# Kernel optimization log

Hardware: AMD Instinct MI355X
Metric: run time of the kernel (lower is better)

## Reference

```python
import jax, jax.numpy as jnp
import numpy as np

INDIM = 1024
NHEADS = 16
DK = INDIM // NHEADS  # 64
DV = INDIM // NHEADS  # 64
B, S = 4, 2048


def setup_inputs() -> dict:
    key = jax.random.key(0)
    ks = jax.random.split(key, 5)
    x = jax.random.normal(ks[0], (B, S, INDIM), dtype=jnp.float32)
    std_qk = np.sqrt(2.0 / (INDIM + DK)).astype(np.float32)
    std_v = np.sqrt(2.0 / (INDIM + DV)).astype(np.float32)
    Wq = jax.random.normal(ks[1], (NHEADS * DK, INDIM), dtype=jnp.float32) * std_qk
    Wk = jax.random.normal(ks[2], (NHEADS * DK, INDIM), dtype=jnp.float32) * std_qk
    Wv = jax.random.normal(ks[3], (NHEADS * DV, INDIM), dtype=jnp.float32) * std_v
    # xavier normal for output proj
    std_o = np.sqrt(2.0 / (NHEADS * DV + INDIM)).astype(np.float32)
    Wo = jax.random.normal(ks[4], (INDIM, NHEADS * DV), dtype=jnp.float32) * std_o
    bq = jnp.zeros((NHEADS * DK,), jnp.float32)
    bk = jnp.zeros((NHEADS * DK,), jnp.float32)
    bv = jnp.zeros((NHEADS * DV,), jnp.float32)
    bo = jnp.zeros((INDIM,), jnp.float32)
    return {"x": x, "Wq": Wq, "bq": bq, "Wk": Wk, "bk": bk, "Wv": Wv, "bv": bv, "Wo": Wo, "bo": bo}


def reference(x, Wq, bq, Wk, bk, Wv, bv, Wo, bo):
    b, s, _ = x.shape
    q = (x @ Wq.T + bq).reshape(b, s, NHEADS, DK)
    k = (x @ Wk.T + bk).reshape(b, s, NHEADS, DK)
    v = (x @ Wv.T + bv).reshape(b, s, NHEADS, DV)
    # scores: [b, h, s, z]
    w = jnp.einsum('bshd,bzhd->bhsz', q, k)
    # original divides by sqrt(d_v) (v.size(-1)) when scale=True
    w = w / jnp.sqrt(jnp.float32(DV))
    w = jax.nn.softmax(w, axis=-1)
    vw = jnp.einsum('bhsz,bzhd->bshd', w, v)  # [b, s, h, dv]
    vw = vw.reshape(b, s, NHEADS * DV)
    out = vw @ Wo.T + bo
    return out
```

## Files before the change

kernel.cpp:

```cpp
#include <hip/hip_runtime.h>
#include <hip/hip_bf16.h>
#include <cstdint>
#include <cstddef>

#define NHEADS 16
#define HDIM   64
#define SEQ    2048
#define BATCH  4
#define IND    1024
#define MTOT   (BATCH*SEQ)

typedef __attribute__((ext_vector_type(8))) short bf16x8;
typedef __attribute__((ext_vector_type(8))) _Float16 f16x8;
typedef __attribute__((ext_vector_type(2))) _Float16 f16x2;
typedef __attribute__((ext_vector_type(4))) float f32x4;
typedef __attribute__((ext_vector_type(16))) float f32x16;
typedef __attribute__((ext_vector_type(2))) int i32x2;
typedef __attribute__((ext_vector_type(4))) unsigned u32x4;

#if __has_builtin(__builtin_amdgcn_exp2f)
#define EXP2(x) __builtin_amdgcn_exp2f(x)
#else
#define EXP2(x) exp2f(x)
#endif

__device__ __forceinline__ unsigned short f2b(float f) {
  unsigned u = __builtin_bit_cast(unsigned, f);
  u += 0x7FFFu + ((u >> 16) & 1u);
  return (unsigned short)(u >> 16);
}
__device__ __forceinline__ unsigned cvt2(float lo, float hi) {
  float2 t; t.x = lo; t.y = hi;
  __hip_bfloat162 h = __float22bfloat162_rn(t);
  const unsigned short ulo = __bfloat16_as_ushort(h.x);
  const unsigned short uhi = __bfloat16_as_ushort(h.y);
  return (unsigned)ulo | ((unsigned)uhi << 16);
}
__device__ __forceinline__ float m3(float a, float b, float c) {
  return fmaxf(fmaxf(a, b), c);
}

__device__ __forceinline__ void gload_lds16(const void* g, void* l) {
  __builtin_amdgcn_global_load_lds(
      (const __attribute__((address_space(1))) void*)g,
      (__attribute__((address_space(3))) void*)l, 16, 0, 0);
}

__global__ void cvt_kernel(const float* __restrict__ src,
                           unsigned short* __restrict__ dst, int n4) {
  int i = blockIdx.x * blockDim.x + threadIdx.x;
  const int stride = gridDim.x * blockDim.x;
  for (; i < n4; i += stride) {
    const float4 v = reinterpret_cast<const float4*>(src)[i];
    ushort4 o;
    o.x = f2b(v.x); o.y = f2b(v.y); o.z = f2b(v.z); o.w = f2b(v.w);
    reinterpret_cast<ushort4*>(dst)[i] = o;
  }
}

__global__ void cvtw_kernel(const float* __restrict__ w0, const float* __restrict__ w1,
                            const float* __restrict__ w2, const float* __restrict__ w3,
                            unsigned short* __restrict__ o0, unsigned short* __restrict__ o1,
                            unsigned short* __restrict__ o2, unsigned short* __restrict__ o3,
                            int n4) {
  const int z = blockIdx.y;
  const float* src = (z == 0) ? w0 : (z == 1) ? w1 : (z == 2) ? w2 : w3;
  unsigned short* dst = (z == 0) ? o0 : (z == 1) ? o1 : (z == 2) ? o2 : o3;
  int i = blockIdx.x * blockDim.x + threadIdx.x;
  const int stride = gridDim.x * blockDim.x;
  for (; i < n4; i += stride) {
    const float4 v = reinterpret_cast<const float4*>(src)[i];
    ushort4 o;
    o.x = f2b(v.x); o.y = f2b(v.y); o.z = f2b(v.z); o.w = f2b(v.w);
    reinterpret_cast<ushort4*>(dst)[i] = o;
  }
}

template<int EPI>
__device__ __forceinline__ void gemm_core(
    const unsigned short* __restrict__ A,
    const unsigned short* __restrict__ Bw,
    const float* __restrict__ bias,
    void* __restrict__ Cout, float scale)
{
  __shared__ alignas(16) unsigned short As[2][4096];
  __shared__ alignas(16) unsigned short Bs[2][4096];
  const int tid = threadIdx.x;
  const int wv = tid >> 6, lane = tid & 63, g = lane >> 4, li = lane & 15;
  const int wr = (wv >> 1) * 64, wc = (wv & 1) * 64;
  const int m0 = blockIdx.x * 128, n0 = blockIdx.y * 128;

  auto stage = [&](int buf, int kt) {
    const int k0 = kt * 32;
#pragma unroll
    for (int rnd = 0; rnd < 2; ++rnd) {
      const int f = (tid + rnd * 256) * 8;
      const int row = f >> 5, col = f & 31;
      gload_lds16(&A[(size_t)(m0 + row) * IND + k0 + col], &As[buf][f]);
      gload_lds16(&Bw[(size_t)(n0 + row) * IND + k0 + col], &Bs[buf][f]);
    }
  };

  f32x4 acc[4][4] = {};
  stage(0, 0);
  for (int kt = 0; kt < 32; ++kt) {
    __syncthreads();
    if (kt + 1 < 32) stage((kt + 1) & 1, kt + 1);
    const int buf = kt & 1;
    bf16x8 af[4], bfr[4];
#pragma unroll
    for (int i = 0; i < 4; ++i)
      af[i] = *(const bf16x8*)&As[buf][(wr + i * 16 + li) * 32 + g * 8];
#pragma unroll
    for (int i = 0; i < 4; ++i)
      bfr[i] = *(const bf16x8*)&Bs[buf][(wc + i * 16 + li) * 32 + g * 8];
#pragma unroll
    for (int mi = 0; mi < 4; ++mi)
#pragma unroll
      for (int ni = 0; ni < 4; ++ni)
        acc[mi][ni] = __builtin_amdgcn_mfma_f32_16x16x32_bf16(
            af[mi], bfr[ni], acc[mi][ni], 0, 0, 0);
  }

#pragma unroll
  for (int ni = 0; ni < 4; ++ni) {
    const int col = n0 + wc + ni * 16 + li;
    const float bz = bias[col];
#pragma unroll
    for (int mi = 0; mi < 4; ++mi) {
#pragma unroll
      for (int r = 0; r < 4; ++r) {
        const int row = m0 + wr + mi * 16 + g * 4 + r;
        float v = acc[mi][ni][r] + bz;
        if (EPI == 0) {
          v *= scale;
          const int h = col >> 6, d = col & 63;
          const int b = row >> 11, s = row & 2047;
          ((unsigned short*)Cout)[(((size_t)(b * NHEADS + h)) * SEQ + s) * HDIM + d] = f2b(v);
        } else if (EPI == 2) {
          const int h = col >> 6, d = col & 63;
          const int b = row >> 11, s = row & 2047;
          ((_Float16*)Cout)[(((size_t)(b * NHEADS + h)) * HDIM + d) * SEQ + s] = (_Float16)v;
        } else {
          ((float*)Cout)[(size_t)row * IND + col] = v;
        }
      }
    }
  }
}

__global__ __launch_bounds__(256, 2)
void gemm_qkv_kernel(const unsigned short* __restrict__ xb,
                     const unsigned short* __restrict__ Wq,
                     const unsigned short* __restrict__ Wk,
                     const unsigned short* __restrict__ Wv,
                     const float* __restrict__ bq,
                     const float* __restrict__ bk,
                     const float* __restrict__ bv,
                     unsigned short* __restrict__ Qo,
                     unsigned short* __restrict__ Ko,
                     unsigned short* __restrict__ Vto)
{
  const int z = blockIdx.z;
  if (z == 2) {
    gemm_core<2>(xb, Wv, bv, Vto, 1.0f);
  } else {
    const unsigned short* Bw = (z == 0) ? Wq : Wk;
    const float* bias = (z == 0) ? bq : bk;
    unsigned short* out = (z == 0) ? Qo : Ko;
    const float scale = (z == 0) ? 0.18033688011111772f : 1.0f;
    gemm_core<0>(xb, Bw, bias, out, scale);
  }
}

__global__ __launch_bounds__(256, 2)
void gemm_o_kernel(const unsigned short* __restrict__ Ab,
                   const unsigned short* __restrict__ Wo,
                   const float* __restrict__ bo,
                   float* __restrict__ out)
{
  gemm_core<1>(Ab, Wo, bo, out, 1.0f);
}

__global__ __launch_bounds__(256, 4)
void attn_kernel(const unsigned short* __restrict__ Q,
                 const unsigned short* __restrict__ K,
                 const unsigned short* __restrict__ Vt,
                 unsigned short* __restrict__ O)
{
  __shared__ alignas(16) unsigned short Kb[2][64 * 64];
  __shared__ alignas(16) unsigned short Vb[2][64 * 64];

  const int tid = threadIdx.x;
  const int wv = tid >> 6, lane = tid & 63;
  const int r31 = lane & 31, hi = lane >> 5;

  const unsigned flat = blockIdx.x;
  const unsigned wg = (flat & 7) * 128 + (flat >> 3);
  const int qblk = wg & 15;
  const int bh = wg >> 4;

  const size_t hbase = (size_t)bh * (SEQ * HDIM);
  const unsigned short* Qh = Q + hbase;
  const unsigned short* Kh = K + hbase;
  const unsigned short* Vh = Vt + hbase;
  const int q0 = qblk * 128 + wv * 32;

  bf16x8 qf[4];
#pragma unroll
  for (int kc = 0; kc < 4; ++kc)
    qf[kc] = *(const bf16x8*)&Qh[(size_t)(q0 + r31) * HDIM + kc * 16 + hi * 8];

  f16x8 onesA;
  {
    const _Float16 ov = (r31 == 0) ? (_Float16)1.0f : (_Float16)0.0f;
#pragma unroll
    for (int j = 0; j < 8; ++j) onesA[j] = ov;
  }

  f32x16 accO[2] = {};
  f32x16 accL = {};
  float m_run = -INFINITY;

  auto stage = [&](int buf, int kv) {
    const int k0 = kv * 64;
#pragma unroll
    for (int rnd = 0; rnd < 2; ++rnd) {
      const int c = tid + rnd * 256;
      const int row = c >> 3, pch = c & 7;
      const int ch = pch ^ (row & 7);
      gload_lds16(&Kh[(size_t)(k0 + row) * HDIM + ch * 8], &Kb[buf][c * 8]);
      gload_lds16(&Vh[(size_t)row * SEQ + k0 + ch * 8], &Vb[buf][c * 8]);
    }
  };

  stage(0, 0);

  for (int kv = 0; kv < SEQ / 64; ++kv) {
    __syncthreads();
    if (kv + 1 < SEQ / 64) stage((kv + 1) & 1, kv + 1);
    const int buf = kv & 1;

    f32x16 s0 = {}, s1 = {};
#pragma unroll
    for (int kc = 0; kc < 4; ++kc) {
      const int pch = (kc * 2 + hi) ^ (r31 & 7);
      const int base = r31 * 64 + pch * 8;
      const bf16x8 kf0 = *(const bf16x8*)&Kb[buf][base];
      s0 = __builtin_amdgcn_mfma_f32_32x32x16_bf16(kf0, qf[kc], s0, 0, 0, 0);
      const bf16x8 kf1 = *(const bf16x8*)&Kb[buf][base + 2048];
      s1 = __builtin_amdgcn_mfma_f32_32x32x16_bf16(kf1, qf[kc], s1, 0, 0, 0);
    }

    float t0 = m3(s0[0], s0[1], s0[2]),   t1 = m3(s0[3], s0[4], s0[5]);
    float t2 = m3(s0[6], s0[7], s0[8]),   t3 = m3(s0[9], s0[10], s0[11]);
    float t4 = m3(s0[12], s0[13], s0[14]);
    float u0 = m3(t0, t1, s0[15]),        u1 = fmaxf(t2, fmaxf(t3, t4));
    float t5 = m3(s1[0], s1[1], s1[2]),   t6 = m3(s1[3], s1[4], s1[5]);
    float t7 = m3(s1[6], s1[7], s1[8]),   t8 = m3(s1[9], s1[10], s1[11]);
    float t9 = m3(s1[12], s1[13], s1[14]);
    float u2 = m3(t5, t6, s1[15]),        u3 = fmaxf(t7, fmaxf(t8, t9));
    float pmax = m3(fmaxf(u0, u1), u2, u3);
    pmax = fmaxf(pmax, __shfl_xor(pmax, 32));

    if (!__all(pmax - m_run <= 8.0f)) {
      const float mn = fmaxf(m_run, pmax);
      const float al = EXP2(m_run - mn);
#pragma unroll
      for (int f = 0; f < 2; ++f)
#pragma unroll
        for (int r = 0; r < 16; ++r) accO[f][r] *= al;
      accL[0] *= al;
      m_run = mn;
    }

    unsigned pk[16];
#pragma unroll
    for (int i = 0; i < 8; ++i) {
      const float ea = EXP2(s0[2 * i] - m_run);
      const float eb = EXP2(s0[2 * i + 1] - m_run);
      pk[i] = __builtin_bit_cast(unsigned, __builtin_amdgcn_cvt_pkrtz(ea, eb));
    }
#pragma unroll
    for (int i = 0; i < 8; ++i) {
      const float ea = EXP2(s1[2 * i] - m_run);
      const float eb = EXP2(s1[2 * i + 1] - m_run);
      pk[8 + i] = __builtin_bit_cast(unsigned, __builtin_amdgcn_cvt_pkrtz(ea, eb));
    }

    f16x8 pf[4];
#pragma unroll
    for (int kc2 = 0; kc2 < 4; ++kc2) {
      const int bs = kc2 * 4;
      const i32x2 rA = __builtin_amdgcn_permlane32_swap(
          (int)pk[bs + 0], (int)pk[bs + 2], false, false);
      const i32x2 rB = __builtin_amdgcn_permlane32_swap(
          (int)pk[bs + 1], (int)pk[bs + 3], false, false);
      u32x4 u;
      u[0] = (unsigned)rA[0];
      u[1] = (unsigned)rB[0];
      u[2] = (unsigned)rA[1];
      u[3] = (unsigned)rB[1];
      pf[kc2] = __builtin_bit_cast(f16x8, u);
    }

#pragma unroll
    for (int kc2 = 0; kc2 < 4; ++kc2) {
      const int pch = (kc2 * 2 + hi) ^ (r31 & 7);
      const int vbase = r31 * 64 + pch * 8;
      const f16x8 vf0 = *(const f16x8*)&Vb[buf][vbase];
      accO[0] = __builtin_amdgcn_mfma_f32_32x32x16_f16(vf0, pf[kc2], accO[0], 0, 0, 0);
      const f16x8 vf1 = *(const f16x8*)&Vb[buf][vbase + 2048];
      accO[1] = __builtin_amdgcn_mfma_f32_32x32x16_f16(vf1, pf[kc2], accO[1], 0, 0, 0);
      accL = __builtin_amdgcn_mfma_f32_32x32x16_f16(onesA, pf[kc2], accL, 0, 0, 0);
    }
  }

  float lv = accL[0];
  lv += __shfl_xor(lv, 32);

  const int b = bh >> 4, h = bh & 15;
  const float inv = 1.0f / lv;
  const int qrow = q0 + r31;
  unsigned short* obase = (unsigned short*)&O[((size_t)(b * SEQ + qrow)) * IND + h * HDIM];
#pragma unroll
  for (int f = 0; f < 2; ++f) {
#pragma unroll
    for (int half = 0; half < 4; ++half) {
      uint2 w;
      w.x = cvt2(accO[f][half * 4 + 0] * inv, accO[f][half * 4 + 1] * inv);
      w.y = cvt2(accO[f][half * 4 + 2] * inv, accO[f][half * 4 + 3] * inv);
      *(uint2*)&obase[32 * f + 8 * half + 4 * hi] = w;
    }
  }
}

extern "C" void kernel_launch(void* const* d_in, const int* in_sizes, int n_in,
                              void* d_out, int out_size, void* d_ws, size_t ws_size,
                              hipStream_t stream) {
  const float* x  = (const float*)d_in[0];
  const float* Wq = (const float*)d_in[1];
  const float* bq = (const float*)d_in[2];
  const float* Wk = (const float*)d_in[3];
  const float* bk = (const float*)d_in[4];
  const float* Wv = (const float*)d_in[5];
  const float* bv = (const float*)d_in[6];
  const float* Wo = (const float*)d_in[7];
  const float* bo = (const float*)d_in[8];

  char* ws = (char*)d_ws;
  constexpr size_t SZ_XB = (size_t)MTOT * IND * 2;
  constexpr size_t SZ_W  = (size_t)IND * IND * 2;
  unsigned short* xb   = (unsigned short*)(ws);
  unsigned short* Wqb  = (unsigned short*)(ws + SZ_XB);
  unsigned short* Wkb  = (unsigned short*)(ws + SZ_XB + SZ_W);
  unsigned short* Wvb  = (unsigned short*)(ws + SZ_XB + 2 * SZ_W);
  unsigned short* Wob  = (unsigned short*)(ws + SZ_XB + 3 * SZ_W);
  unsigned short* Qb   = (unsigned short*)(ws + SZ_XB + 4 * SZ_W);
  unsigned short* Kbuf = (unsigned short*)(ws + 2 * SZ_XB + 4 * SZ_W);
  unsigned short* Vtb  = (unsigned short*)(ws + 3 * SZ_XB + 4 * SZ_W);
  unsigned short* AOb  = (unsigned short*)(ws + 4 * SZ_XB + 4 * SZ_W);

  cvt_kernel<<<2048, 256, 0, stream>>>(x, xb, (MTOT * IND) / 4);
  cvtw_kernel<<<dim3(512, 4), 256, 0, stream>>>(Wq, Wk, Wv, Wo,
                                                Wqb, Wkb, Wvb, Wob, (IND * IND) / 4);

  gemm_qkv_kernel<<<dim3(MTOT / 128, IND / 128, 3), 256, 0, stream>>>(
      xb, Wqb, Wkb, Wvb, bq, bk, bv, Qb, Kbuf, Vtb);

  attn_kernel<<<dim3(16 * BATCH * NHEADS), 256, 0, stream>>>(Qb, Kbuf, Vtb, AOb);

  gemm_o_kernel<<<dim3(MTOT / 128, IND / 128), 256, 0, stream>>>(
      AOb, Wob, bo, (float*)d_out);
}
```

Before: 207.3 us.

## Split attention KV range in two with combine kernel; transpose V-projection MFMA epilogue

New measurement: 406.5 us. +96.1%, slower.

```diff
diff --git a/kernel.cpp b/kernel.cpp
--- a/kernel.cpp
+++ b/kernel.cpp
@@ -12,7 +12,6 @@
 
 typedef __attribute__((ext_vector_type(8))) short bf16x8;
 typedef __attribute__((ext_vector_type(8))) _Float16 f16x8;
-typedef __attribute__((ext_vector_type(2))) _Float16 f16x2;
 typedef __attribute__((ext_vector_type(4))) float f32x4;
 typedef __attribute__((ext_vector_type(16))) float f32x16;
 typedef __attribute__((ext_vector_type(2))) int i32x2;
@@ -35,6 +34,9 @@
   const unsigned short ulo = __bfloat16_as_ushort(h.x);
   const unsigned short uhi = __bfloat16_as_ushort(h.y);
   return (unsigned)ulo | ((unsigned)uhi << 16);
+}
+__device__ __forceinline__ unsigned pkrtz(float lo, float hi) {
+  return __builtin_bit_cast(unsigned, __builtin_amdgcn_cvt_pkrtz(lo, hi));
 }
 __device__ __forceinline__ float m3(float a, float b, float c) {
   return fmaxf(fmaxf(a, b), c);
@@ -117,32 +119,53 @@
 #pragma unroll
     for (int mi = 0; mi < 4; ++mi)
 #pragma unroll
-      for (int ni = 0; ni < 4; ++ni)
-        acc[mi][ni] = __builtin_amdgcn_mfma_f32_16x16x32_bf16(
-            af[mi], bfr[ni], acc[mi][ni], 0, 0, 0);
-  }
-
-#pragma unroll
-  for (int ni = 0; ni < 4; ++ni) {
-    const int col = n0 + wc + ni * 16 + li;
-    const float bz = bias[col];
-#pragma unroll
-    for (int mi = 0; mi < 4; ++mi) {
+      for (int ni = 0; ni < 4; ++ni) {
+        if (EPI == 2)
+          acc[mi][ni] = __builtin_amdgcn_mfma_f32_16x16x32_bf16(
+              bfr[ni], af[mi], acc[mi][ni], 0, 0, 0);
+        else
+          acc[mi][ni] = __builtin_amdgcn_mfma_f32_16x16x32_bf16(
+              af[mi], bfr[ni], acc[mi][ni], 0, 0, 0);
+      }
+  }
+
+  if (EPI == 2) {
+#pragma unroll
+    for (int ni = 0; ni < 4; ++ni) {
 #pragma unroll
       for (int r = 0; r < 4; ++r) {
-        const int row = m0 + wr + mi * 16 + g * 4 + r;
-        float v = acc[mi][ni][r] + bz;
-        if (EPI == 0) {
-          v *= scale;
-          const int h = col >> 6, d = col & 63;
-          const int b = row >> 11, s = row & 2047;
-          ((unsigned short*)Cout)[(((size_t)(b * NHEADS + h)) * SEQ + s) * HDIM + d] = f2b(v);
-        } else if (EPI == 2) {
-          const int h = col >> 6, d = col & 63;
-          const int b = row >> 11, s = row & 2047;
-          ((_Float16*)Cout)[(((size_t)(b * NHEADS + h)) * HDIM + d) * SEQ + s] = (_Float16)v;
-        } else {
-          ((float*)Cout)[(size_t)row * IND + col] = v;
+        const int n = n0 + wc + ni * 16 + g * 4 + r;
+        const float bz = bias[n];
+        const int h = n >> 6, d = n & 63;
+#pragma unroll
+        for (int mi = 0; mi < 4; ++mi) {
+          const int tok = m0 + wr + mi * 16 + li;
+          const int b = tok >> 11, s = tok & 2047;
+          const float v = acc[mi][ni][r] + bz;
+          ((_Float16*)Cout)[(((size_t)(b * NHEADS + h)) * HDIM + d) * SEQ + s] =
+              (_Float16)v;
+        }
+      }
+    }
+  } else {
+#pragma unroll
+    for (int ni = 0; ni < 4; ++ni) {
+      const int col = n0 + wc + ni * 16 + li;
+      const float bz = bias[col];
+#pragma unroll
+      for (int mi = 0; mi < 4; ++mi) {
+#pragma unroll
+        for (int r = 0; r < 4; ++r) {
+          const int row = m0 + wr + mi * 16 + g * 4 + r;
+          float v = acc[mi][ni][r] + bz;
+          if (EPI == 0) {
+            v *= scale;
+            const int h = col >> 6, d = col & 63;
+            const int b = row >> 11, s = row & 2047;
+            ((unsigned short*)Cout)[(((size_t)(b * NHEADS + h)) * SEQ + s) * HDIM + d] = f2b(v);
+          } else {
+            ((float*)Cout)[(size_t)row * IND + col] = v;
+          }
         }
       }
     }
@@ -182,23 +205,28 @@
   gemm_core<1>(Ab, Wo, bo, out, 1.0f);
 }
 
-__global__ __launch_bounds__(256, 4)
+__global__ __launch_bounds__(256, 8)
 void attn_kernel(const unsigned short* __restrict__ Q,
                  const unsigned short* __restrict__ K,
                  const unsigned short* __restrict__ Vt,
-                 unsigned short* __restrict__ O)
+                 unsigned short* __restrict__ U0,
+                 unsigned short* __restrict__ U1,
+                 float* __restrict__ Ml,
+                 float* __restrict__ Ll)
 {
-  __shared__ alignas(16) unsigned short Kb[2][64 * 64];
-  __shared__ alignas(16) unsigned short Vb[2][64 * 64];
+  __shared__ alignas(16) unsigned short Kb[2][32 * 64];
+  __shared__ alignas(16) unsigned short Vb[2][64 * 32];
 
   const int tid = threadIdx.x;
   const int wv = tid >> 6, lane = tid & 63;
   const int r31 = lane & 31, hi = lane >> 5;
 
   const unsigned flat = blockIdx.x;
-  const unsigned wg = (flat & 7) * 128 + (flat >> 3);
+  const unsigned wg = (flat & 7) * 256 + (flat >> 3);
   const int qblk = wg & 15;
-  const int bh = wg >> 4;
+  const int bh = (wg >> 4) & 63;
+  const int split = wg >> 10;
+  const int koff = split * 1024;
 
   const size_t hbase = (size_t)bh * (SEQ * HDIM);
   const unsigned short* Qh = Q + hbase;
@@ -211,86 +239,70 @@
   for (int kc = 0; kc < 4; ++kc)
     qf[kc] = *(const bf16x8*)&Qh[(size_t)(q0 + r31) * HDIM + kc * 16 + hi * 8];
 
-  f16x8 onesA;
-  {
-    const _Float16 ov = (r31 == 0) ? (_Float16)1.0f : (_Float16)0.0f;
-#pragma unroll
-    for (int j = 0; j < 8; ++j) onesA[j] = ov;
-  }
-
   f32x16 accO[2] = {};
-  f32x16 accL = {};
-  float m_run = -INFINITY;
+  float m_run = -INFINITY, l_run = 0.0f;
 
   auto stage = [&](int buf, int kv) {
-    const int k0 = kv * 64;
-#pragma unroll
-    for (int rnd = 0; rnd < 2; ++rnd) {
-      const int c = tid + rnd * 256;
-      const int row = c >> 3, pch = c & 7;
+    const int k0 = koff + kv * 32;
+    {
+      const int row = tid >> 3, pch = tid & 7;
       const int ch = pch ^ (row & 7);
-      gload_lds16(&Kh[(size_t)(k0 + row) * HDIM + ch * 8], &Kb[buf][c * 8]);
-      gload_lds16(&Vh[(size_t)row * SEQ + k0 + ch * 8], &Vb[buf][c * 8]);
+      gload_lds16(&Kh[(size_t)(k0 + row) * HDIM + ch * 8], &Kb[buf][tid * 8]);
+    }
+    {
+      const int row = tid >> 2, pch = tid & 3;
+      const int ch = pch ^ ((row >> 1) & 3);
+      gload_lds16(&Vh[(size_t)row * SEQ + k0 + ch * 8], &Vb[buf][tid * 8]);
     }
   };
 
   stage(0, 0);
 
-  for (int kv = 0; kv < SEQ / 64; ++kv) {
+  for (int kv = 0; kv < 32; ++kv) {
     __syncthreads();
-    if (kv + 1 < SEQ / 64) stage((kv + 1) & 1, kv + 1);
+    if (kv + 1 < 32) stage((kv + 1) & 1, kv + 1);
     const int buf = kv & 1;
 
-    f32x16 s0 = {}, s1 = {};
+    f32x16 s0 = {};
 #pragma unroll
     for (int kc = 0; kc < 4; ++kc) {
       const int pch = (kc * 2 + hi) ^ (r31 & 7);
-      const int base = r31 * 64 + pch * 8;
-      const bf16x8 kf0 = *(const bf16x8*)&Kb[buf][base];
-      s0 = __builtin_amdgcn_mfma_f32_32x32x16_bf16(kf0, qf[kc], s0, 0, 0, 0);
-      const bf16x8 kf1 = *(const bf16x8*)&Kb[buf][base + 2048];
-      s1 = __builtin_amdgcn_mfma_f32_32x32x16_bf16(kf1, qf[kc], s1, 0, 0, 0);
-    }
-
-    float t0 = m3(s0[0], s0[1], s0[2]),   t1 = m3(s0[3], s0[4], s0[5]);
-    float t2 = m3(s0[6], s0[7], s0[8]),   t3 = m3(s0[9], s0[10], s0[11]);
+      const bf16x8 kf = *(const bf16x8*)&Kb[buf][r31 * 64 + pch * 8];
+      s0 = __builtin_amdgcn_mfma_f32_32x32x16_bf16(kf, qf[kc], s0, 0, 0, 0);
+    }
+
+    float t0 = m3(s0[0], s0[1], s0[2]),  t1 = m3(s0[3], s0[4], s0[5]);
+    float t2 = m3(s0[6], s0[7], s0[8]),  t3 = m3(s0[9], s0[10], s0[11]);
     float t4 = m3(s0[12], s0[13], s0[14]);
-    float u0 = m3(t0, t1, s0[15]),        u1 = fmaxf(t2, fmaxf(t3, t4));
-    float t5 = m3(s1[0], s1[1], s1[2]),   t6 = m3(s1[3], s1[4], s1[5]);
-    float t7 = m3(s1[6], s1[7], s1[8]),   t8 = m3(s1[9], s1[10], s1[11]);
-    float t9 = m3(s1[12], s1[13], s1[14]);
-    float u2 = m3(t5, t6, s1[15]),        u3 = fmaxf(t7, fmaxf(t8, t9));
-    float pmax = m3(fmaxf(u0, u1), u2, u3);
+    float pmax = m3(m3(t0, t1, s0[15]), fmaxf(t2, t3), t4);
     pmax = fmaxf(pmax, __shfl_xor(pmax, 32));
 
     if (!__all(pmax - m_run <= 8.0f)) {
       const float mn = fmaxf(m_run, pmax);
       const float al = EXP2(m_run - mn);
+      l_run *= al;
 #pragma unroll
       for (int f = 0; f < 2; ++f)
 #pragma unroll
         for (int r = 0; r < 16; ++r) accO[f][r] *= al;
-      accL[0] *= al;
       m_run = mn;
     }
 
-    unsigned pk[16];
+    unsigned pk[8];
+    float rs = 0.0f;
 #pragma unroll
     for (int i = 0; i < 8; ++i) {
       const float ea = EXP2(s0[2 * i] - m_run);
       const float eb = EXP2(s0[2 * i + 1] - m_run);
-      pk[i] = __builtin_bit_cast(unsigned, __builtin_amdgcn_cvt_pkrtz(ea, eb));
-    }
-#pragma unroll
-    for (int i = 0; i < 8; ++i) {
-      const float ea = EXP2(s1[2 * i] - m_run);
-      const float eb = EXP2(s1[2 * i + 1] - m_run);
-      pk[8 + i] = __builtin_bit_cast(unsigned, __builtin_amdgcn_cvt_pkrtz(ea, eb));
-    }
-
-    f16x8 pf[4];
-#pragma unroll
-    for (int kc2 = 0; kc2 < 4; ++kc2) {
+      rs += ea + eb;
+      pk[i] = pkrtz(ea, eb);
+    }
+    rs += __shfl_xor(rs, 32);
+    l_run += rs;
+
+    f16x8 pf[2];
+#pragma unroll
+    for (int kc2 = 0; kc2 < 2; ++kc2) {
       const int bs = kc2 * 4;
       const i32x2 rA = __builtin_amdgcn_permlane32_swap(
           (int)pk[bs + 0], (int)pk[bs + 2], false, false);
@@ -305,33 +317,71 @@
     }
 
 #pragma unroll
-    for (int kc2 = 0; kc2 < 4; ++kc2) {
-      const int pch = (kc2 * 2 + hi) ^ (r31 & 7);
-      const int vbase = r31 * 64 + pch * 8;
+    for (int kc2 = 0; kc2 < 2; ++kc2) {
+      const int vpch = (kc2 * 2 + hi) ^ ((r31 >> 1) & 3);
+      const int vbase = r31 * 32 + vpch * 8;
       const f16x8 vf0 = *(const f16x8*)&Vb[buf][vbase];
       accO[0] = __builtin_amdgcn_mfma_f32_32x32x16_f16(vf0, pf[kc2], accO[0], 0, 0, 0);
-      const f16x8 vf1 = *(const f16x8*)&Vb[buf][vbase + 2048];
+      const f16x8 vf1 = *(const f16x8*)&Vb[buf][vbase + 1024];
       accO[1] = __builtin_amdgcn_mfma_f32_32x32x16_f16(vf1, pf[kc2], accO[1], 0, 0, 0);
-      accL = __builtin_amdgcn_mfma_f32_32x32x16_f16(onesA, pf[kc2], accL, 0, 0, 0);
-    }
-  }
-
-  float lv = accL[0];
-  lv += __shfl_xor(lv, 32);
+    }
+  }
 
   const int b = bh >> 4, h = bh & 15;
-  const float inv = 1.0f / lv;
   const int qrow = q0 + r31;
-  unsigned short* obase = (unsigned short*)&O[((size_t)(b * SEQ + qrow)) * IND + h * HDIM];
+  unsigned short* Up = (split == 0) ? U0 : U1;
+  unsigned short* obase = &Up[((size_t)(b * SEQ + qrow)) * IND + h * HDIM];
 #pragma unroll
   for (int f = 0; f < 2; ++f) {
 #pragma unroll
     for (int half = 0; half < 4; ++half) {
       uint2 w;
-      w.x = cvt2(accO[f][half * 4 + 0] * inv, accO[f][half * 4 + 1] * inv);
-      w.y = cvt2(accO[f][half * 4 + 2] * inv, accO[f][half * 4 + 3] * inv);
+      w.x = pkrtz(accO[f][half * 4 + 0], accO[f][half * 4 + 1]);
+      w.y = pkrtz(accO[f][half * 4 + 2], accO[f][half * 4 + 3]);
       *(uint2*)&obase[32 * f + 8 * half + 4 * hi] = w;
     }
+  }
+  if (hi == 0) {
+    Ml[((size_t)(split * 64 + bh)) * SEQ + qrow] = m_run;
+    Ll[((size_t)(split * 64 + bh)) * SEQ + qrow] = l_run;
+  }
+}
+
+__global__ __launch_bounds__(256, 8)
+void combine_kernel(const unsigned short* U0h,
+                    const unsigned short* __restrict__ U1h,
+                    const float* __restrict__ Ml, const float* __restrict__ Ll,
+                    unsigned short* O)
+{
+  const int bh = blockIdx.x;
+  const int q0 = blockIdx.y * 128;
+  const int tid = threadIdx.x;
+  const int qq = q0 + (tid >> 1);
+  const int dh = (tid & 1) * 32;
+  const int b = bh >> 4, h = bh & 15;
+
+  const float m0v = Ml[(size_t)bh * SEQ + qq];
+  const float m1v = Ml[(size_t)(64 + bh) * SEQ + qq];
+  const float l0 = Ll[(size_t)bh * SEQ + qq];
+  const float l1 = Ll[(size_t)(64 + bh) * SEQ + qq];
+  const float mm = fmaxf(m0v, m1v);
+  const float a0 = EXP2(m0v - mm), a1 = EXP2(m1v - mm);
+  const float inv = 1.0f / (l0 * a0 + l1 * a1);
+  const float c0 = a0 * inv, c1 = a1 * inv;
+
+  const size_t base = ((size_t)(b * SEQ + qq)) * IND + h * HDIM + dh;
+#pragma unroll
+  for (int it = 0; it < 4; ++it) {
+    const f16x8 u0 = *(const f16x8*)&U0h[base + it * 8];
+    const f16x8 u1 = *(const f16x8*)&U1h[base + it * 8];
+    float o[8];
+#pragma unroll
+    for (int j = 0; j < 8; ++j)
+      o[j] = (float)u0[j] * c0 + (float)u1[j] * c1;
+    uint4 w;
+    w.x = cvt2(o[0], o[1]); w.y = cvt2(o[2], o[3]);
+    w.z = cvt2(o[4], o[5]); w.w = cvt2(o[6], o[7]);
+    *(uint4*)&O[base + it * 8] = w;
   }
 }
 
@@ -361,6 +411,10 @@
   unsigned short* Vtb  = (unsigned short*)(ws + 3 * SZ_XB + 4 * SZ_W);
   unsigned short* AOb  = (unsigned short*)(ws + 4 * SZ_XB + 4 * SZ_W);
 
+  unsigned short* U1   = xb;
+  float*          Mlp  = (float*)Wqb;
+  float*          Llp  = (float*)Wkb;
+
   cvt_kernel<<<2048, 256, 0, stream>>>(x, xb, (MTOT * IND) / 4);
   cvtw_kernel<<<dim3(512, 4), 256, 0, stream>>>(Wq, Wk, Wv, Wo,
                                                 Wqb, Wkb, Wvb, Wob, (IND * IND) / 4);
@@ -368,7 +422,10 @@
   gemm_qkv_kernel<<<dim3(MTOT / 128, IND / 128, 3), 256, 0, stream>>>(
       xb, Wqb, Wkb, Wvb, bq, bk, bv, Qb, Kbuf, Vtb);
 
-  attn_kernel<<<dim3(16 * BATCH * NHEADS), 256, 0, stream>>>(Qb, Kbuf, Vtb, AOb);
+  attn_kernel<<<dim3(2048), 256, 0, stream>>>(Qb, Kbuf, Vtb, AOb, U1, Mlp, Llp);
+
+  combine_kernel<<<dim3(BATCH * NHEADS, SEQ / 128), 256, 0, stream>>>(
+      AOb, U1, Mlp, Llp, AOb);
 
   gemm_o_kernel<<<dim3(MTOT / 128, IND / 128), 256, 0, stream>>>(
       AOb, Wob, bo, (float*)d_out);
```
